# Performance work log

Measured on AMD Instinct MI355X. Metric: run time of the kernel, lower is better.

The kernel has to match this reference:

```python
import jax, jax.numpy as jnp
import numpy as np

N_NODES = 100000
N_EDGES = 1000000
D_IN, D_HID, D_OUT = 64, 64, 64


def _glorot(key, shape):
    fan_in, fan_out = shape[1], shape[0]
    lim = (6.0 / (fan_in + fan_out)) ** 0.5
    return jax.random.uniform(key, shape, jnp.float32, -lim, lim)


def setup_inputs() -> dict:
    key = jax.random.key(0)
    ks = jax.random.split(key, 8)
    x = jax.random.normal(ks[0], (N_NODES, D_IN), dtype=jnp.float32)
    edge_index = jax.random.randint(ks[1], (2, N_EDGES), 0, N_NODES, dtype=jnp.int64)
    # SAGEConv params: lin_l (applied to aggregated neighbors, has bias), lin_r (root, no bias)
    W1l = _glorot(ks[2], (D_HID, D_IN)); b1l = jnp.zeros((D_HID,), jnp.float32)
    W1r = _glorot(ks[3], (D_HID, D_IN))
    W2l = _glorot(ks[4], (D_OUT, D_HID)); b2l = jnp.zeros((D_OUT,), jnp.float32)
    W2r = _glorot(ks[5], (D_OUT, D_HID))
    return {"x": x, "edge_index": edge_index,
            "W1l": W1l, "b1l": b1l, "W1r": W1r,
            "W2l": W2l, "b2l": b2l, "W2r": W2r}


def _sage_conv(x, src, dst, Wl, bl, Wr, num_nodes):
    # gather source features, scatter-mean onto destinations
    msg = x[src]                                        # [E, d]
    agg = jax.ops.segment_sum(msg, dst, num_segments=num_nodes)   # [N, d]
    cnt = jax.ops.segment_sum(jnp.ones((src.shape[0],), x.dtype), dst,
                              num_segments=num_nodes)   # [N]
    mean = agg / jnp.maximum(cnt, 1.0)[:, None]
    # out = lin_l(mean_neighbors) + lin_r(x)
    return mean @ Wl.T + bl + x @ Wr.T


def reference(x, edge_index, W1l, b1l, W1r, W2l, b2l, W2r):
    src, dst = edge_index[0], edge_index[1]
    n = x.shape[0]
    h = jax.nn.relu(_sage_conv(x, src, dst, W1l, b1l, W1r, n))
    out = _sage_conv(h, src, dst, W2l, b2l, W2r, n)
    return out
```

## Files before the change

### kernel.cpp

```cpp
#include <hip/hip_runtime.h>

#define N_NODES 100000
#define N_EDGES 1000000
#define D 64
#define NB 196
#define SUBCAP 1024
#define BSTAGE 6144
#define CHUNK 4096
#define ABLOCKS ((N_EDGES + CHUNK - 1) / CHUNK)
#define NTILES (N_NODES / 16)
#define FB 768
#define FW (FB * 4)

typedef __attribute__((ext_vector_type(8))) __bf16 bf16x8;
typedef __attribute__((ext_vector_type(4))) float f32x4;

__device__ __forceinline__ unsigned short f2b(float f) {
    unsigned u = __float_as_uint(f);
    unsigned r = u + 0x7FFFu + ((u >> 16) & 1u);
    return (unsigned short)(r >> 16);
}
__device__ __forceinline__ float blo(unsigned u) {
    return __uint_as_float(u << 16);
}
__device__ __forceinline__ float bhi(unsigned u) {
    return __uint_as_float(u & 0xFFFF0000u);
}
__device__ __forceinline__ unsigned pack2(float a, float b) {
    return (unsigned)f2b(a) | ((unsigned)f2b(b) << 16);
}

__device__ __forceinline__ void split8(float4 p, float4 q, uint4& hv, uint4& lv) {
    float e[8] = {p.x, p.y, p.z, p.w, q.x, q.y, q.z, q.w};
    unsigned hb[8], lb[8];
#pragma unroll
    for (int i = 0; i < 8; i++) {
        unsigned u = __float_as_uint(e[i]);
        unsigned hf = u & 0xFFFF0000u;
        hb[i] = u >> 16;
        lb[i] = f2b(e[i] - __uint_as_float(hf));
    }
    hv.x = hb[0] | (hb[1] << 16); hv.y = hb[2] | (hb[3] << 16);
    hv.z = hb[4] | (hb[5] << 16); hv.w = hb[6] | (hb[7] << 16);
    lv.x = lb[0] | (lb[1] << 16); lv.y = lb[2] | (lb[3] << 16);
    lv.z = lb[4] | (lb[5] << 16); lv.w = lb[6] | (lb[7] << 16);
}

__global__ void __launch_bounds__(256)
k_bucketA(const int* __restrict__ ei, int* __restrict__ subcur,
          int* __restrict__ pairs) {
    __shared__ int hist[256];
    __shared__ int sc[256];
    __shared__ int lpos[NB];
    __shared__ int lcur[NB];
    __shared__ int gbase[NB];
    __shared__ int stage[CHUNK];
    __shared__ int astage[CHUNK];
    int t = threadIdx.x, blk = blockIdx.x;
    int sub = blk & 7;
    int e0 = blk * CHUNK;
    int e1 = min(e0 + CHUNK, N_EDGES);
    int cnt = e1 - e0;

    hist[t] = 0;
    __syncthreads();
    for (int i = t; i < cnt; i += 256) {
        int d = ei[N_EDGES + e0 + i];
        atomicAdd(&hist[d >> 9], 1);
    }
    __syncthreads();
    int h = hist[t];
    sc[t] = h;
    __syncthreads();
    for (int off = 1; off < 256; off <<= 1) {
        int v = (t >= off) ? sc[t - off] : 0;
        __syncthreads();
        sc[t] += v;
        __syncthreads();
    }
    if (t < NB) {
        int excl = sc[t] - h;
        lpos[t] = excl;
        lcur[t] = excl;
        gbase[t] = (h > 0) ? atomicAdd(&subcur[(t << 3) | sub], h) : 0;
    }
    __syncthreads();
    for (int i = t; i < cnt; i += 256) {
        int s = ei[e0 + i];
        int d = ei[N_EDGES + e0 + i];
        int b = d >> 9;
        int p = atomicAdd(&lcur[b], 1);
        int o = gbase[b] + (p - lpos[b]);
        stage[p] = (s << 9) | (d & 511);
        astage[p] = (o < SUBCAP) ? (((b << 3) | sub) * SUBCAP + o) : -1;
    }
    __syncthreads();
    for (int i = t; i < cnt; i += 256) {
        int a = astage[i];
        if (a >= 0) pairs[a] = stage[i];
    }
}

__global__ void k_bscan(const int* __restrict__ subcur, int* __restrict__ bucket_base) {
    __shared__ int tot[256];
    int t = threadIdx.x;
    int sum = 0;
    if (t < NB) {
        for (int s = 0; s < 8; s++) sum += min(subcur[t * 8 + s], SUBCAP);
    }
    tot[t] = sum;
    __syncthreads();
    for (int off = 1; off < 256; off <<= 1) {
        int v = (t >= off) ? tot[t - off] : 0;
        __syncthreads();
        tot[t] += v;
        __syncthreads();
    }
    if (t < NB) bucket_base[t] = (t == 0) ? 0 : tot[t - 1];
    if (t == NB - 1) bucket_base[NB] = tot[t];
}

__global__ void __launch_bounds__(256)
k_bucketB(const int* __restrict__ subcur, const int* __restrict__ pairs,
          const int* __restrict__ bucket_base, int* __restrict__ col,
          int* __restrict__ row_start, float* __restrict__ invc) {
    __shared__ int ldeg[512];
    __shared__ int lpos[512];
    __shared__ int lcur[512];
    __shared__ int sc[256];
    __shared__ int cnt[8];
    __shared__ int stage[BSTAGE];
    int b = blockIdx.x, t = threadIdx.x;
    if (t < 8) cnt[t] = min(subcur[b * 8 + t], SUBCAP);
    for (int i = t; i < 512; i += 256) ldeg[i] = 0;
    __syncthreads();
    for (int s = 0; s < 8; s++) {
        int c = cnt[s];
        const int* base = pairs + (size_t)(b * 8 + s) * SUBCAP;
        for (int i = t; i < c; i += 256) atomicAdd(&ldeg[base[i] & 511], 1);
    }
    __syncthreads();
    int a0 = ldeg[2 * t], a1 = ldeg[2 * t + 1];
    sc[t] = a0 + a1;
    __syncthreads();
    for (int off = 1; off < 256; off <<= 1) {
        int v = (t >= off) ? sc[t - off] : 0;
        __syncthreads();
        sc[t] += v;
        __syncthreads();
    }
    int excl = (t == 0) ? 0 : sc[t - 1];
    lpos[2 * t] = excl;
    lpos[2 * t + 1] = excl + a0;
    lcur[2 * t] = excl;
    lcur[2 * t + 1] = excl + a0;
    __syncthreads();
    int bbase = bucket_base[b];
    int total = bucket_base[b + 1] - bbase;
    if (total > BSTAGE) total = BSTAGE;
    int n0 = b * 512;
    for (int i = t; i < 512; i += 256) {
        int n = n0 + i;
        if (n < N_NODES) {
            row_start[n] = bbase + lpos[i];
            int dg = ldeg[i];
            invc[n] = 1.0f / (float)(dg > 0 ? dg : 1);
        }
    }
    if (b == 0 && t == 0) row_start[N_NODES] = bucket_base[NB];
    for (int s = 0; s < 8; s++) {
        int c = cnt[s];
        const int* base = pairs + (size_t)(b * 8 + s) * SUBCAP;
        for (int i = t; i < c; i += 256) {
            int v = base[i];
            int p = atomicAdd(&lcur[v & 511], 1);
            if (p < BSTAGE) stage[p] = v >> 9;
        }
    }
    __syncthreads();
    for (int i = t; i < total; i += 256) col[bbase + i] = stage[i];
}

__global__ void __launch_bounds__(256)
k_cast(const float4* __restrict__ X4, uint4* __restrict__ Xb) {
    int i = blockIdx.x * 256 + threadIdx.x;
    if (i >= N_NODES * D / 8) return;
    float4 a = X4[2 * i];
    float4 b = X4[2 * i + 1];
    uint4 o;
    o.x = pack2(a.x, a.y);
    o.y = pack2(a.z, a.w);
    o.z = pack2(b.x, b.y);
    o.w = pack2(b.z, b.w);
    Xb[i] = o;
}

__device__ __forceinline__ void lin_tile(
    const uint4 ahv[4], const uint4 alv[4],
    const uint4 (*wHp)[4][64], const uint4 (*wLp)[4][64],
    const float4 bq[4], int lane, int kg, size_t n,
    float* __restrict__ out, unsigned* __restrict__ xb_out, int do_relu)
{
    f32x4 acc[4];
#pragma unroll
    for (int ot = 0; ot < 4; ot++) {
        f32x4 a;
        a[0] = bq[ot].x; a[1] = bq[ot].y; a[2] = bq[ot].z; a[3] = bq[ot].w;
        acc[ot] = a;
    }
#pragma unroll
    for (int kb = 0; kb < 4; kb++) {
        bf16x8 ah = __builtin_bit_cast(bf16x8, ahv[kb]);
        bf16x8 al = __builtin_bit_cast(bf16x8, alv[kb]);
#pragma unroll
        for (int ot = 0; ot < 4; ot++) {
            bf16x8 wh = __builtin_bit_cast(bf16x8, wHp[kb][ot][lane]);
            bf16x8 wl = __builtin_bit_cast(bf16x8, wLp[kb][ot][lane]);
            acc[ot] = __builtin_amdgcn_mfma_f32_16x16x32_bf16(wh, ah, acc[ot], 0, 0, 0);
            acc[ot] = __builtin_amdgcn_mfma_f32_16x16x32_bf16(wh, al, acc[ot], 0, 0, 0);
            acc[ot] = __builtin_amdgcn_mfma_f32_16x16x32_bf16(wl, ah, acc[ot], 0, 0, 0);
        }
    }
#pragma unroll
    for (int ot = 0; ot < 4; ot++) {
        float v0 = acc[ot][0], v1 = acc[ot][1], v2 = acc[ot][2], v3 = acc[ot][3];
        if (do_relu) {
            v0 = fmaxf(v0, 0.f); v1 = fmaxf(v1, 0.f);
            v2 = fmaxf(v2, 0.f); v3 = fmaxf(v3, 0.f);
        }
        *(float4*)(out + n * 64 + ot * 16 + kg * 4) = make_float4(v0, v1, v2, v3);
        if (xb_out) {
            *(uint2*)(xb_out + n * 32 + ot * 8 + kg * 2) =
                make_uint2(pack2(v0, v1), pack2(v2, v3));
        }
    }
}

__global__ void __launch_bounds__(256, 3)
k_agg_lin(const uint4* __restrict__ Xb, const float* __restrict__ Xa,
          const int* __restrict__ row_start, const int* __restrict__ col,
          const float* __restrict__ invc,
          const float* __restrict__ Wl, const float* __restrict__ Wr,
          const float* __restrict__ bias, float* __restrict__ out,
          int do_relu, unsigned* __restrict__ xb_out) {
    __shared__ uint4 wH[4][4][64];
    __shared__ uint4 wL[4][4][64];
    __shared__ float mrow[4][16 * 68];
    int t = threadIdx.x;

    for (int idx = t; idx < 1024; idx += 256) {
        int lane = idx & 63;
        int ot = (idx >> 6) & 3;
        int kb = idx >> 8;
        int oc = ot * 16 + (lane & 15);
        int kk = kb * 32 + (lane >> 4) * 8;
        const float* src = (kk < 64) ? (Wl + oc * 64 + kk)
                                     : (Wr + oc * 64 + (kk - 64));
        float4 p = *(const float4*)src;
        float4 q = *(const float4*)(src + 4);
        uint4 hv, lv;
        split8(p, q, hv, lv);
        wH[kb][ot][lane] = hv;
        wL[kb][ot][lane] = lv;
    }
    __syncthreads();

    int lane = t & 63;
    int wv = t >> 6;
    int nin = lane & 15;
    int kg = lane >> 4;
    int na = lane >> 2;
    int sub4 = lane & 3;
    float* ms = mrow[wv];

    float4 bq[4];
#pragma unroll
    for (int ot = 0; ot < 4; ot++)
        bq[ot] = *(const float4*)(bias + ot * 16 + kg * 4);

    int w = blockIdx.x * 4 + wv;
    int t0 = (w * 7) % FW;
    for (int tile = t0; tile < NTILES; tile += FW) {
        int nagg = tile * 16 + na;
        int s = row_start[nagg];
        int e = row_start[nagg + 1];
        float ic = invc[nagg];
        size_t nlin = (size_t)tile * 16 + nin;

        const float4* xp = (const float4*)Xa + nlin * 16 + kg * 2;
        float4 x0 = xp[0], x1 = xp[1], x2 = xp[8], x3 = xp[9];

        float a[16];
#pragma unroll
        for (int i = 0; i < 16; i++) a[i] = 0.f;
        int cb = 2 * sub4;
        int j = s;
        for (; j + 4 <= e; j += 4) {
            int c0 = col[j + 0], c1 = col[j + 1], c2 = col[j + 2], c3 = col[j + 3];
            uint4 q0a = Xb[(size_t)c0 * 8 + cb], q0b = Xb[(size_t)c0 * 8 + cb + 1];
            uint4 q1a = Xb[(size_t)c1 * 8 + cb], q1b = Xb[(size_t)c1 * 8 + cb + 1];
            uint4 q2a = Xb[(size_t)c2 * 8 + cb], q2b = Xb[(size_t)c2 * 8 + cb + 1];
            uint4 q3a = Xb[(size_t)c3 * 8 + cb], q3b = Xb[(size_t)c3 * 8 + cb + 1];
            const unsigned* u0a = (const unsigned*)&q0a;
            const unsigned* u1a = (const unsigned*)&q1a;
            const unsigned* u2a = (const unsigned*)&q2a;
            const unsigned* u3a = (const unsigned*)&q3a;
            const unsigned* u0b = (const unsigned*)&q0b;
            const unsigned* u1b = (const unsigned*)&q1b;
            const unsigned* u2b = (const unsigned*)&q2b;
            const unsigned* u3b = (const unsigned*)&q3b;
#pragma unroll
            for (int wd = 0; wd < 4; wd++) {
                a[2 * wd + 0] += (blo(u0a[wd]) + blo(u1a[wd])) + (blo(u2a[wd]) + blo(u3a[wd]));
                a[2 * wd + 1] += (bhi(u0a[wd]) + bhi(u1a[wd])) + (bhi(u2a[wd]) + bhi(u3a[wd]));
                a[8 + 2 * wd + 0] += (blo(u0b[wd]) + blo(u1b[wd])) + (blo(u2b[wd]) + blo(u3b[wd]));
                a[8 + 2 * wd + 1] += (bhi(u0b[wd]) + bhi(u1b[wd])) + (bhi(u2b[wd]) + bhi(u3b[wd]));
            }
        }
        for (; j < e; j++) {
            int c = col[j];
            uint4 qa = Xb[(size_t)c * 8 + cb], qb = Xb[(size_t)c * 8 + cb + 1];
            const unsigned* ua = (const unsigned*)&qa;
            const unsigned* ub = (const unsigned*)&qb;
#pragma unroll
            for (int wd = 0; wd < 4; wd++) {
                a[2 * wd + 0] += blo(ua[wd]);
                a[2 * wd + 1] += bhi(ua[wd]);
                a[8 + 2 * wd + 0] += blo(ub[wd]);
                a[8 + 2 * wd + 1] += bhi(ub[wd]);
            }
        }

        int wb = na * 68 + sub4 * 16;
#pragma unroll
        for (int i4 = 0; i4 < 4; i4++) {
            *(float4*)&ms[wb + i4 * 4] = make_float4(a[i4 * 4 + 0] * ic, a[i4 * 4 + 1] * ic,
                                                     a[i4 * 4 + 2] * ic, a[i4 * 4 + 3] * ic);
        }
        asm volatile("s_waitcnt lgkmcnt(0)" ::: "memory");
        __builtin_amdgcn_sched_barrier(0);

        uint4 ahv[4], alv[4];
        {
            int rb = nin * 68 + kg * 8;
            float4 m0 = *(const float4*)&ms[rb + 0];
            float4 m1 = *(const float4*)&ms[rb + 4];
            float4 m2 = *(const float4*)&ms[rb + 32];
            float4 m3 = *(const float4*)&ms[rb + 36];
            split8(m0, m1, ahv[0], alv[0]);
            split8(m2, m3, ahv[1], alv[1]);
        }
        split8(x0, x1, ahv[2], alv[2]);
        split8(x2, x3, ahv[3], alv[3]);

        lin_tile(ahv, alv, wH, wL, bq, lane, kg, nlin, out, xb_out, do_relu);
    }
}

extern "C" void kernel_launch(void* const* d_in, const int* in_sizes, int n_in,
                              void* d_out, int out_size, void* d_ws, size_t ws_size,
                              hipStream_t stream) {
    const float* x   = (const float*)d_in[0];
    const int*   ei  = (const int*)d_in[1];
    const float* W1l = (const float*)d_in[2];
    const float* b1  = (const float*)d_in[3];
    const float* W1r = (const float*)d_in[4];
    const float* W2l = (const float*)d_in[5];
    const float* b2  = (const float*)d_in[6];
    const float* W2r = (const float*)d_in[7];
    float* out = (float*)d_out;

    char* ws = (char*)d_ws;
    size_t off = 0;
    auto alloc = [&](size_t bytes) -> char* {
        char* p = ws + off;
        off = (off + bytes + 255) & ~(size_t)255;
        return p;
    };
    int*   row_start   = (int*)alloc((size_t)(N_NODES + 1) * 4);
    int*   col         = (int*)alloc((size_t)N_EDGES * 4);
    float* invc        = (float*)alloc((size_t)N_NODES * 4);
    int*   subcur      = (int*)alloc((size_t)NB * 8 * 4);
    int*   bucket_base = (int*)alloc((size_t)(NB + 1) * 4);
    char*  region      = alloc((size_t)N_NODES * D * 2);
    char*  xb2region   = alloc((size_t)N_NODES * D * 2);
    float* hbuf        = (float*)alloc((size_t)N_NODES * D * 4);
    int*   pairs = (int*)region;
    uint4* xb    = (uint4*)region;
    uint4* xb2   = (uint4*)xb2region;

    hipMemsetAsync(subcur, 0, (size_t)NB * 8 * 4, stream);
    k_bucketA<<<ABLOCKS, 256, 0, stream>>>(ei, subcur, pairs);
    k_bscan<<<1, 256, 0, stream>>>(subcur, bucket_base);
    k_bucketB<<<NB, 256, 0, stream>>>(subcur, pairs, bucket_base, col, row_start, invc);

    const int cast_blocks = (N_NODES * D / 8 + 255) / 256;

    k_cast<<<cast_blocks, 256, 0, stream>>>((const float4*)x, xb);
    k_agg_lin<<<FB, 256, 0, stream>>>(xb, x, row_start, col, invc,
                                      W1l, W1r, b1, hbuf, 1, (unsigned*)xb2);
    k_agg_lin<<<FB, 256, 0, stream>>>(xb2, hbuf, row_start, col, invc,
                                      W2l, W2r, b2, out, 0, nullptr);
}
```

Before: 204.9 us.

## Process tile pairs with interleaved gathers and atomic work-stealing scheduler

Each wavefront now takes two 16-node tiles at a time and interleaves the neighbor gathers for both, so more independent memory loads are in flight to hide latency. A global atomic counter replaces the static strided tile assignment to balance uneven degree distributions across waves. This raises register pressure under the 3-blocks-per-CU launch bound and adds one atomic per pair. The counters are zeroed by the existing memset.

```diff
diff --git a/kernel.cpp b/kernel.cpp
--- a/kernel.cpp
+++ b/kernel.cpp
@@ -9,8 +9,8 @@
 #define CHUNK 4096
 #define ABLOCKS ((N_EDGES + CHUNK - 1) / CHUNK)
 #define NTILES (N_NODES / 16)
+#define NPAIRS (NTILES / 2)
 #define FB 768
-#define FW (FB * 4)
 
 typedef __attribute__((ext_vector_type(8))) __bf16 bf16x8;
 typedef __attribute__((ext_vector_type(4))) float f32x4;
@@ -236,13 +236,53 @@
     }
 }
 
+__device__ __forceinline__ void acc4(const uint4* __restrict__ Xb,
+                                     const int* __restrict__ col, int j, int cb,
+                                     float* a) {
+    int c0 = col[j + 0], c1 = col[j + 1], c2 = col[j + 2], c3 = col[j + 3];
+    uint4 q0a = Xb[(size_t)c0 * 8 + cb], q0b = Xb[(size_t)c0 * 8 + cb + 1];
+    uint4 q1a = Xb[(size_t)c1 * 8 + cb], q1b = Xb[(size_t)c1 * 8 + cb + 1];
+    uint4 q2a = Xb[(size_t)c2 * 8 + cb], q2b = Xb[(size_t)c2 * 8 + cb + 1];
+    uint4 q3a = Xb[(size_t)c3 * 8 + cb], q3b = Xb[(size_t)c3 * 8 + cb + 1];
+    const unsigned* u0a = (const unsigned*)&q0a;
+    const unsigned* u1a = (const unsigned*)&q1a;
+    const unsigned* u2a = (const unsigned*)&q2a;
+    const unsigned* u3a = (const unsigned*)&q3a;
+    const unsigned* u0b = (const unsigned*)&q0b;
+    const unsigned* u1b = (const unsigned*)&q1b;
+    const unsigned* u2b = (const unsigned*)&q2b;
+    const unsigned* u3b = (const unsigned*)&q3b;
+#pragma unroll
+    for (int wd = 0; wd < 4; wd++) {
+        a[2 * wd + 0] += (blo(u0a[wd]) + blo(u1a[wd])) + (blo(u2a[wd]) + blo(u3a[wd]));
+        a[2 * wd + 1] += (bhi(u0a[wd]) + bhi(u1a[wd])) + (bhi(u2a[wd]) + bhi(u3a[wd]));
+        a[8 + 2 * wd + 0] += (blo(u0b[wd]) + blo(u1b[wd])) + (blo(u2b[wd]) + blo(u3b[wd]));
+        a[8 + 2 * wd + 1] += (bhi(u0b[wd]) + bhi(u1b[wd])) + (bhi(u2b[wd]) + bhi(u3b[wd]));
+    }
+}
+__device__ __forceinline__ void acc1(const uint4* __restrict__ Xb,
+                                     const int* __restrict__ col, int j, int cb,
+                                     float* a) {
+    int c = col[j];
+    uint4 qa = Xb[(size_t)c * 8 + cb], qb = Xb[(size_t)c * 8 + cb + 1];
+    const unsigned* ua = (const unsigned*)&qa;
+    const unsigned* ub = (const unsigned*)&qb;
+#pragma unroll
+    for (int wd = 0; wd < 4; wd++) {
+        a[2 * wd + 0] += blo(ua[wd]);
+        a[2 * wd + 1] += bhi(ua[wd]);
+        a[8 + 2 * wd + 0] += blo(ub[wd]);
+        a[8 + 2 * wd + 1] += bhi(ub[wd]);
+    }
+}
+
 __global__ void __launch_bounds__(256, 3)
 k_agg_lin(const uint4* __restrict__ Xb, const float* __restrict__ Xa,
           const int* __restrict__ row_start, const int* __restrict__ col,
           const float* __restrict__ invc,
           const float* __restrict__ Wl, const float* __restrict__ Wr,
           const float* __restrict__ bias, float* __restrict__ out,
-          int do_relu, unsigned* __restrict__ xb_out) {
+          int do_relu, unsigned* __restrict__ xb_out, int* __restrict__ ctr) {
     __shared__ uint4 wH[4][4][64];
     __shared__ uint4 wL[4][4][64];
     __shared__ float mrow[4][16 * 68];
@@ -271,6 +311,7 @@
     int kg = lane >> 4;
     int na = lane >> 2;
     int sub4 = lane & 3;
+    int cb = 2 * sub4;
     float* ms = mrow[wv];
 
     float4 bq[4];
@@ -278,68 +319,82 @@
     for (int ot = 0; ot < 4; ot++)
         bq[ot] = *(const float4*)(bias + ot * 16 + kg * 4);
 
-    int w = blockIdx.x * 4 + wv;
-    int t0 = (w * 7) % FW;
-    for (int tile = t0; tile < NTILES; tile += FW) {
-        int nagg = tile * 16 + na;
-        int s = row_start[nagg];
-        int e = row_start[nagg + 1];
-        float ic = invc[nagg];
-        size_t nlin = (size_t)tile * 16 + nin;
-
-        const float4* xp = (const float4*)Xa + nlin * 16 + kg * 2;
-        float4 x0 = xp[0], x1 = xp[1], x2 = xp[8], x3 = xp[9];
-
-        float a[16];
-#pragma unroll
-        for (int i = 0; i < 16; i++) a[i] = 0.f;
-        int cb = 2 * sub4;
-        int j = s;
-        for (; j + 4 <= e; j += 4) {
-            int c0 = col[j + 0], c1 = col[j + 1], c2 = col[j + 2], c3 = col[j + 3];
-            uint4 q0a = Xb[(size_t)c0 * 8 + cb], q0b = Xb[(size_t)c0 * 8 + cb + 1];
-            uint4 q1a = Xb[(size_t)c1 * 8 + cb], q1b = Xb[(size_t)c1 * 8 + cb + 1];
-            uint4 q2a = Xb[(size_t)c2 * 8 + cb], q2b = Xb[(size_t)c2 * 8 + cb + 1];
-            uint4 q3a = Xb[(size_t)c3 * 8 + cb], q3b = Xb[(size_t)c3 * 8 + cb + 1];
-            const unsigned* u0a = (const unsigned*)&q0a;
-            const unsigned* u1a = (const unsigned*)&q1a;
-            const unsigned* u2a = (const unsigned*)&q2a;
-            const unsigned* u3a = (const unsigned*)&q3a;
-            const unsigned* u0b = (const unsigned*)&q0b;
-            const unsigned* u1b = (const unsigned*)&q1b;
-            const unsigned* u2b = (const unsigned*)&q2b;
-            const unsigned* u3b = (const unsigned*)&q3b;
+    for (;;) {
+        int p;
+        if (lane == 0) p = atomicAdd(ctr, 1);
+        p = __shfl(p, 0, 64);
+        if (p >= NPAIRS) break;
+        int tile0 = 2 * p, tile1 = 2 * p + 1;
+
+        int nA = tile0 * 16 + na;
+        int nB = tile1 * 16 + na;
+        int sA = row_start[nA], eA = row_start[nA + 1];
+        int sB = row_start[nB], eB = row_start[nB + 1];
+        float icA = invc[nA], icB = invc[nB];
+        size_t nlin0 = (size_t)tile0 * 16 + nin;
+        size_t nlin1 = (size_t)tile1 * 16 + nin;
+
+        const float4* xp0 = (const float4*)Xa + nlin0 * 16 + kg * 2;
+        float4 x00 = xp0[0], x01 = xp0[1], x02 = xp0[8], x03 = xp0[9];
+
+        float aA[16], aB[16];
+#pragma unroll
+        for (int i = 0; i < 16; i++) { aA[i] = 0.f; aB[i] = 0.f; }
+
+        int jA = sA, jB = sB;
+        while (jA + 4 <= eA && jB + 4 <= eB) {
+            int cA0 = col[jA + 0], cA1 = col[jA + 1], cA2 = col[jA + 2], cA3 = col[jA + 3];
+            int cB0 = col[jB + 0], cB1 = col[jB + 1], cB2 = col[jB + 2], cB3 = col[jB + 3];
+            uint4 qA0a = Xb[(size_t)cA0 * 8 + cb], qA0b = Xb[(size_t)cA0 * 8 + cb + 1];
+            uint4 qA1a = Xb[(size_t)cA1 * 8 + cb], qA1b = Xb[(size_t)cA1 * 8 + cb + 1];
+            uint4 qA2a = Xb[(size_t)cA2 * 8 + cb], qA2b = Xb[(size_t)cA2 * 8 + cb + 1];
+            uint4 qA3a = Xb[(size_t)cA3 * 8 + cb], qA3b = Xb[(size_t)cA3 * 8 + cb + 1];
+            uint4 qB0a = Xb[(size_t)cB0 * 8 + cb], qB0b = Xb[(size_t)cB0 * 8 + cb + 1];
+            uint4 qB1a = Xb[(size_t)cB1 * 8 + cb], qB1b = Xb[(size_t)cB1 * 8 + cb + 1];
+            uint4 qB2a = Xb[(size_t)cB2 * 8 + cb], qB2b = Xb[(size_t)cB2 * 8 + cb + 1];
+            uint4 qB3a = Xb[(size_t)cB3 * 8 + cb], qB3b = Xb[(size_t)cB3 * 8 + cb + 1];
+            const unsigned* uA0a = (const unsigned*)&qA0a;
+            const unsigned* uA1a = (const unsigned*)&qA1a;
+            const unsigned* uA2a = (const unsigned*)&qA2a;
+            const unsigned* uA3a = (const unsigned*)&qA3a;
+            const unsigned* uA0b = (const unsigned*)&qA0b;
+            const unsigned* uA1b = (const unsigned*)&qA1b;
+            const unsigned* uA2b = (const unsigned*)&qA2b;
+            const unsigned* uA3b = (const unsigned*)&qA3b;
+            const unsigned* uB0a = (const unsigned*)&qB0a;
+            const unsigned* uB1a = (const unsigned*)&qB1a;
+            const unsigned* uB2a = (const unsigned*)&qB2a;
+            const unsigned* uB3a = (const unsigned*)&qB3a;
+            const unsigned* uB0b = (const unsigned*)&qB0b;
+            const unsigned* uB1b = (const unsigned*)&qB1b;
+            const unsigned* uB2b = (const unsigned*)&qB2b;
+            const unsigned* uB3b = (const unsigned*)&qB3b;
 #pragma unroll
             for (int wd = 0; wd < 4; wd++) {
-                a[2 * wd + 0] += (blo(u0a[wd]) + blo(u1a[wd])) + (blo(u2a[wd]) + blo(u3a[wd]));
-                a[2 * wd + 1] += (bhi(u0a[wd]) + bhi(u1a[wd])) + (bhi(u2a[wd]) + bhi(u3a[wd]));
-                a[8 + 2 * wd + 0] += (blo(u0b[wd]) + blo(u1b[wd])) + (blo(u2b[wd]) + blo(u3b[wd]));
-                a[8 + 2 * wd + 1] += (bhi(u0b[wd]) + bhi(u1b[wd])) + (bhi(u2b[wd]) + bhi(u3b[wd]));
+                aA[2 * wd + 0] += (blo(uA0a[wd]) + blo(uA1a[wd])) + (blo(uA2a[wd]) + blo(uA3a[wd]));
+                aA[2 * wd + 1] += (bhi(uA0a[wd]) + bhi(uA1a[wd])) + (bhi(uA2a[wd]) + bhi(uA3a[wd]));
+                aA[8 + 2 * wd + 0] += (blo(uA0b[wd]) + blo(uA1b[wd])) + (blo(uA2b[wd]) + blo(uA3b[wd]));
+                aA[8 + 2 * wd + 1] += (bhi(uA0b[wd]) + bhi(uA1b[wd])) + (bhi(uA2b[wd]) + bhi(uA3b[wd]));
+                aB[2 * wd + 0] += (blo(uB0a[wd]) + blo(uB1a[wd])) + (blo(uB2a[wd]) + blo(uB3a[wd]));
+                aB[2 * wd + 1] += (bhi(uB0a[wd]) + bhi(uB1a[wd])) + (bhi(uB2a[wd]) + bhi(uB3a[wd]));
+                aB[8 + 2 * wd + 0] += (blo(uB0b[wd]) + blo(uB1b[wd])) + (blo(uB2b[wd]) + blo(uB3b[wd]));
+                aB[8 + 2 * wd + 1] += (bhi(uB0b[wd]) + bhi(uB1b[wd])) + (bhi(uB2b[wd]) + bhi(uB3b[wd]));
             }
-        }
-        for (; j < e; j++) {
-            int c = col[j];
-            uint4 qa = Xb[(size_t)c * 8 + cb], qb = Xb[(size_t)c * 8 + cb + 1];
-            const unsigned* ua = (const unsigned*)&qa;
-            const unsigned* ub = (const unsigned*)&qb;
-#pragma unroll
-            for (int wd = 0; wd < 4; wd++) {
-                a[2 * wd + 0] += blo(ua[wd]);
-                a[2 * wd + 1] += bhi(ua[wd]);
-                a[8 + 2 * wd + 0] += blo(ub[wd]);
-                a[8 + 2 * wd + 1] += bhi(ub[wd]);
-            }
-        }
+            jA += 4; jB += 4;
+        }
+        for (; jA + 4 <= eA; jA += 4) acc4(Xb, col, jA, cb, aA);
+        for (; jA < eA; jA++)         acc1(Xb, col, jA, cb, aA);
+        for (; jB + 4 <= eB; jB += 4) acc4(Xb, col, jB, cb, aB);
+        for (; jB < eB; jB++)         acc1(Xb, col, jB, cb, aB);
 
         int wb = na * 68 + sub4 * 16;
 #pragma unroll
         for (int i4 = 0; i4 < 4; i4++) {
-            *(float4*)&ms[wb + i4 * 4] = make_float4(a[i4 * 4 + 0] * ic, a[i4 * 4 + 1] * ic,
-                                                     a[i4 * 4 + 2] * ic, a[i4 * 4 + 3] * ic);
+            *(float4*)&ms[wb + i4 * 4] = make_float4(aA[i4 * 4 + 0] * icA, aA[i4 * 4 + 1] * icA,
+                                                     aA[i4 * 4 + 2] * icA, aA[i4 * 4 + 3] * icA);
         }
         asm volatile("s_waitcnt lgkmcnt(0)" ::: "memory");
         __builtin_amdgcn_sched_barrier(0);
-
         uint4 ahv[4], alv[4];
         {
             int rb = nin * 68 + kg * 8;
@@ -350,10 +405,33 @@
             split8(m0, m1, ahv[0], alv[0]);
             split8(m2, m3, ahv[1], alv[1]);
         }
-        split8(x0, x1, ahv[2], alv[2]);
-        split8(x2, x3, ahv[3], alv[3]);
-
-        lin_tile(ahv, alv, wH, wL, bq, lane, kg, nlin, out, xb_out, do_relu);
+        const float4* xp1 = (const float4*)Xa + nlin1 * 16 + kg * 2;
+        float4 x10 = xp1[0], x11 = xp1[1], x12 = xp1[8], x13 = xp1[9];
+
+        split8(x00, x01, ahv[2], alv[2]);
+        split8(x02, x03, ahv[3], alv[3]);
+        lin_tile(ahv, alv, wH, wL, bq, lane, kg, nlin0, out, xb_out, do_relu);
+
+        asm volatile("s_waitcnt lgkmcnt(0)" ::: "memory");
+#pragma unroll
+        for (int i4 = 0; i4 < 4; i4++) {
+            *(float4*)&ms[wb + i4 * 4] = make_float4(aB[i4 * 4 + 0] * icB, aB[i4 * 4 + 1] * icB,
+                                                     aB[i4 * 4 + 2] * icB, aB[i4 * 4 + 3] * icB);
+        }
+        asm volatile("s_waitcnt lgkmcnt(0)" ::: "memory");
+        __builtin_amdgcn_sched_barrier(0);
+        {
+            int rb = nin * 68 + kg * 8;
+            float4 m0 = *(const float4*)&ms[rb + 0];
+            float4 m1 = *(const float4*)&ms[rb + 4];
+            float4 m2 = *(const float4*)&ms[rb + 32];
+            float4 m3 = *(const float4*)&ms[rb + 36];
+            split8(m0, m1, ahv[0], alv[0]);
+            split8(m2, m3, ahv[1], alv[1]);
+        }
+        split8(x10, x11, ahv[2], alv[2]);
+        split8(x12, x13, ahv[3], alv[3]);
+        lin_tile(ahv, alv, wH, wL, bq, lane, kg, nlin1, out, xb_out, do_relu);
     }
 }
 
@@ -380,7 +458,7 @@
     int*   row_start   = (int*)alloc((size_t)(N_NODES + 1) * 4);
     int*   col         = (int*)alloc((size_t)N_EDGES * 4);
     float* invc        = (float*)alloc((size_t)N_NODES * 4);
-    int*   subcur      = (int*)alloc((size_t)NB * 8 * 4);
+    int*   subcur      = (int*)alloc((size_t)NB * 8 * 4 + 8);
     int*   bucket_base = (int*)alloc((size_t)(NB + 1) * 4);
     char*  region      = alloc((size_t)N_NODES * D * 2);
     char*  xb2region   = alloc((size_t)N_NODES * D * 2);
@@ -388,8 +466,9 @@
     int*   pairs = (int*)region;
     uint4* xb    = (uint4*)region;
     uint4* xb2   = (uint4*)xb2region;
-
-    hipMemsetAsync(subcur, 0, (size_t)NB * 8 * 4, stream);
+    int*   ctr   = subcur + NB * 8;
+
+    hipMemsetAsync(subcur, 0, (size_t)NB * 8 * 4 + 8, stream);
     k_bucketA<<<ABLOCKS, 256, 0, stream>>>(ei, subcur, pairs);
     k_bscan<<<1, 256, 0, stream>>>(subcur, bucket_base);
     k_bucketB<<<NB, 256, 0, stream>>>(subcur, pairs, bucket_base, col, row_start, invc);
@@ -398,7 +477,7 @@
 
     k_cast<<<cast_blocks, 256, 0, stream>>>((const float4*)x, xb);
     k_agg_lin<<<FB, 256, 0, stream>>>(xb, x, row_start, col, invc,
-                                      W1l, W1r, b1, hbuf, 1, (unsigned*)xb2);
+                                      W1l, W1r, b1, hbuf, 1, (unsigned*)xb2, ctr);
     k_agg_lin<<<FB, 256, 0, stream>>>(xb2, hbuf, row_start, col, invc,
-                                      W2l, W2r, b2, out, 0, nullptr);
-}
+                                      W2l, W2r, b2, out, 0, nullptr, ctr + 1);
+}
```

Measured after the change: 322.7 us. +57.5%, slower.

## Replace LDS transpose with ds_bpermute and raise occupancy of agg-lin kernel

Applied to the files above, without the earlier changes.

Drops the per-wave shared-memory staging buffer for mean rows and moves the aggregated values between lanes with ds_bpermute instead. The gather now assigns feature columns to lanes so that each lane's chunks match the layout the MFMA operands expect. With the LDS footprint reduced, launch bounds rise from 3 to 4 blocks per SIMD and the grid grows to match. In exchange it issues 16 bpermute operations per tile and tightens the register budget, which could cause spills.

```diff
diff --git a/kernel.cpp b/kernel.cpp
--- a/kernel.cpp
+++ b/kernel.cpp
@@ -9,7 +9,7 @@
 #define CHUNK 4096
 #define ABLOCKS ((N_EDGES + CHUNK - 1) / CHUNK)
 #define NTILES (N_NODES / 16)
-#define FB 768
+#define FB 1280
 #define FW (FB * 4)
 
 typedef __attribute__((ext_vector_type(8))) __bf16 bf16x8;
@@ -236,7 +236,7 @@
     }
 }
 
-__global__ void __launch_bounds__(256, 3)
+__global__ void __launch_bounds__(256, 4)
 k_agg_lin(const uint4* __restrict__ Xb, const float* __restrict__ Xa,
           const int* __restrict__ row_start, const int* __restrict__ col,
           const float* __restrict__ invc,
@@ -245,7 +245,6 @@
           int do_relu, unsigned* __restrict__ xb_out) {
     __shared__ uint4 wH[4][4][64];
     __shared__ uint4 wL[4][4][64];
-    __shared__ float mrow[4][16 * 68];
     int t = threadIdx.x;
 
     for (int idx = t; idx < 1024; idx += 256) {
@@ -271,7 +270,7 @@
     int kg = lane >> 4;
     int na = lane >> 2;
     int sub4 = lane & 3;
-    float* ms = mrow[wv];
+    int srcl = ((nin * 4) + kg) << 2;
 
     float4 bq[4];
 #pragma unroll
@@ -293,14 +292,13 @@
         float a[16];
 #pragma unroll
         for (int i = 0; i < 16; i++) a[i] = 0.f;
-        int cb = 2 * sub4;
         int j = s;
         for (; j + 4 <= e; j += 4) {
             int c0 = col[j + 0], c1 = col[j + 1], c2 = col[j + 2], c3 = col[j + 3];
-            uint4 q0a = Xb[(size_t)c0 * 8 + cb], q0b = Xb[(size_t)c0 * 8 + cb + 1];
-            uint4 q1a = Xb[(size_t)c1 * 8 + cb], q1b = Xb[(size_t)c1 * 8 + cb + 1];
-            uint4 q2a = Xb[(size_t)c2 * 8 + cb], q2b = Xb[(size_t)c2 * 8 + cb + 1];
-            uint4 q3a = Xb[(size_t)c3 * 8 + cb], q3b = Xb[(size_t)c3 * 8 + cb + 1];
+            uint4 q0a = Xb[(size_t)c0 * 8 + sub4], q0b = Xb[(size_t)c0 * 8 + 4 + sub4];
+            uint4 q1a = Xb[(size_t)c1 * 8 + sub4], q1b = Xb[(size_t)c1 * 8 + 4 + sub4];
+            uint4 q2a = Xb[(size_t)c2 * 8 + sub4], q2b = Xb[(size_t)c2 * 8 + 4 + sub4];
+            uint4 q3a = Xb[(size_t)c3 * 8 + sub4], q3b = Xb[(size_t)c3 * 8 + 4 + sub4];
             const unsigned* u0a = (const unsigned*)&q0a;
             const unsigned* u1a = (const unsigned*)&q1a;
             const unsigned* u2a = (const unsigned*)&q2a;
@@ -319,7 +317,7 @@
         }
         for (; j < e; j++) {
             int c = col[j];
-            uint4 qa = Xb[(size_t)c * 8 + cb], qb = Xb[(size_t)c * 8 + cb + 1];
+            uint4 qa = Xb[(size_t)c * 8 + sub4], qb = Xb[(size_t)c * 8 + 4 + sub4];
             const unsigned* ua = (const unsigned*)&qa;
             const unsigned* ub = (const unsigned*)&qb;
 #pragma unroll
@@ -331,25 +329,24 @@
             }
         }
 
-        int wb = na * 68 + sub4 * 16;
-#pragma unroll
-        for (int i4 = 0; i4 < 4; i4++) {
-            *(float4*)&ms[wb + i4 * 4] = make_float4(a[i4 * 4 + 0] * ic, a[i4 * 4 + 1] * ic,
-                                                     a[i4 * 4 + 2] * ic, a[i4 * 4 + 3] * ic);
-        }
-        asm volatile("s_waitcnt lgkmcnt(0)" ::: "memory");
-        __builtin_amdgcn_sched_barrier(0);
+        unsigned rr[16];
+#pragma unroll
+        for (int i = 0; i < 16; i++) {
+            rr[i] = (unsigned)__builtin_amdgcn_ds_bpermute(
+                srcl, (int)__float_as_uint(a[i] * ic));
+        }
+        float4 m0 = make_float4(__uint_as_float(rr[0]), __uint_as_float(rr[1]),
+                                __uint_as_float(rr[2]), __uint_as_float(rr[3]));
+        float4 m1 = make_float4(__uint_as_float(rr[4]), __uint_as_float(rr[5]),
+                                __uint_as_float(rr[6]), __uint_as_float(rr[7]));
+        float4 m2 = make_float4(__uint_as_float(rr[8]), __uint_as_float(rr[9]),
+                                __uint_as_float(rr[10]), __uint_as_float(rr[11]));
+        float4 m3 = make_float4(__uint_as_float(rr[12]), __uint_as_float(rr[13]),
+                                __uint_as_float(rr[14]), __uint_as_float(rr[15]));
 
         uint4 ahv[4], alv[4];
-        {
-            int rb = nin * 68 + kg * 8;
-            float4 m0 = *(const float4*)&ms[rb + 0];
-            float4 m1 = *(const float4*)&ms[rb + 4];
-            float4 m2 = *(const float4*)&ms[rb + 32];
-            float4 m3 = *(const float4*)&ms[rb + 36];
-            split8(m0, m1, ahv[0], alv[0]);
-            split8(m2, m3, ahv[1], alv[1]);
-        }
+        split8(m0, m1, ahv[0], alv[0]);
+        split8(m2, m3, ahv[1], alv[1]);
         split8(x0, x1, ahv[2], alv[2]);
         split8(x2, x3, ahv[3], alv[3]);
 
```

Measured after the change: 309.1 us. 50.9% more time.
